# Kernel optimization log

Measured on AMD Instinct MI355X. Metric: run time of the kernel, lower is better.

The kernel has to match this reference:

```python
import jax, jax.numpy as jnp
import numpy as np


def setup_inputs() -> dict:
    key = jax.random.key(0)
    k1, = jax.random.split(key, 1)
    N, H, C, T = 4, 16, 64, 2048
    qkv = jax.random.normal(k1, (N, 3 * H * C, T), dtype=jnp.float32)
    mask = jnp.ones((N, T), dtype=jnp.float32)
    return {"qkv": qkv, "mask": mask, "n_heads": H}


def reference(qkv, mask, n_heads):
    bs, width, length = qkv.shape
    ch = width // (3 * n_heads)
    # [bs*H, 3*ch, T] -> split into q, k, v each [bs*H, ch, T]
    qkv_r = qkv.reshape(bs * n_heads, ch * 3, length)
    q, k, v = qkv_r[:, :ch], qkv_r[:, ch:2 * ch], qkv_r[:, 2 * ch:]
    scale = 1.0 / (ch ** 0.25)  # scale applied to both q and k, as in original
    weight = jnp.einsum('bct,bcs->bts', q * scale, k * scale)  # [bs*H, T, T]
    weight = jax.nn.softmax(weight.astype(jnp.float32), axis=-1).astype(qkv.dtype)
    # torch mask.repeat(n_heads, 1).unsqueeze(1) == tile over leading dim -> [bs*H, 1, T]
    mask_r = jnp.tile(mask, (n_heads, 1))[:, None, :]
    weight = weight * mask_r  # post-softmax multiply (faithful to original)
    a = jnp.einsum('bts,bcs->bct', weight, v)  # [bs*H, ch, T]
    return a.reshape(bs, -1, length)
```

## Files before the change

### kernel.cpp

```cpp
#include <hip/hip_runtime.h>
#include <hip/hip_bf16.h>

typedef __attribute__((ext_vector_type(4))) float f32x4;
typedef __attribute__((ext_vector_type(2))) float f32x2;
typedef __attribute__((ext_vector_type(8))) short s16x8;
typedef __attribute__((ext_vector_type(4))) short s16x4;

constexpr int T_SEQ = 2048;
constexpr int D = 64;
constexpr int H = 16;
constexpr int QBLK = 128;
constexpr int KVBLK = 64;
constexpr int NTHREADS = 512;
constexpr float LOG2E = 1.44269504088896340736f;

__device__ __forceinline__ short f2bf(float f) {
  return (short)__builtin_bit_cast(unsigned short, __float2bfloat16(f));
}

__device__ __forceinline__ float fast_exp2(float x) {
#if __has_builtin(__builtin_amdgcn_exp2f)
  return __builtin_amdgcn_exp2f(x);
#else
  return exp2f(x);
#endif
}

__device__ __forceinline__ int swz(int row, int colByte) {
  return row * 128 + (colByte ^ ((row & 7) << 4));
}

__global__ __launch_bounds__(NTHREADS, 6)
void attn_kernel(const float* __restrict__ qkv, const float* __restrict__ mask,
                 float* __restrict__ out) {
  __shared__ __align__(16) char smem[40960];
  char* Qc = smem;
  char* Kc = smem;
  char* Vc = smem + 8192;
  char* Pc = smem + 16384;
  float* maskLds = (float*)(smem + 32768);

  const int tid = threadIdx.x;
  int flat = blockIdx.y * 16 + blockIdx.x;
  flat = (flat & 7) * 128 + (flat >> 3);
  const int qt = flat & 15;
  const int bh = flat >> 4;
  const int b = bh >> 4, h = bh & 15;

  const size_t headBase = ((size_t)b * (3 * H * D) + (size_t)h * (3 * D)) * T_SEQ;
  const float* gQ = qkv + headBase;
  const float* gK = gQ + (size_t)D * T_SEQ;
  const float* gV = gQ + (size_t)(2 * D) * T_SEQ;
  const float* gM = mask + (size_t)(bh & 3) * T_SEQ;

  *(f32x4*)&maskLds[tid * 4] = *(const f32x4*)&gM[tid * 4];
  {
    const int sb = (tid & 31) * 4;
    const int cb = (tid >> 5) * 4;
    const int q0 = qt * QBLK;
    const float qscale = 0.125f * LOG2E;
    f32x4 r[4];
#pragma unroll
    for (int j = 0; j < 4; ++j)
      r[j] = *(const f32x4*)(gQ + (size_t)(cb + j) * T_SEQ + q0 + sb);
#pragma unroll
    for (int i = 0; i < 4; ++i) {
      s16x4 w;
#pragma unroll
      for (int j = 0; j < 4; ++j) w[j] = f2bf(r[j][i] * qscale);
      *(s16x4*)(Qc + swz(sb + i, 2 * cb)) = w;
    }
  }
  __syncthreads();

  const int wave = tid >> 6, lane = tid & 63;
  const int lg = lane >> 4, lid = lane & 15;

  s16x8 aq[2];
#pragma unroll
  for (int ko = 0; ko < 2; ++ko)
    aq[ko] = *(const s16x8*)(Qc + swz(wave * 16 + lid, 16 * lg + 64 * ko));

  float m0 = -1e30f, l0 = 0.0f;
  f32x4 accO[4];
#pragma unroll
  for (int ct = 0; ct < 4; ++ct) accO[ct] = (f32x4){0.f, 0.f, 0.f, 0.f};

  char* Pw = Pc + wave * 2048;

  for (int s0 = 0; s0 < T_SEQ; s0 += KVBLK) {
    __syncthreads();
    if (tid < 256) {
      const int sb = 2 * (tid & 31);
      const int cb = 8 * (tid >> 5);
      f32x2 r[8];
#pragma unroll
      for (int j = 0; j < 8; ++j)
        r[j] = *(const f32x2*)(gK + (size_t)(cb + j) * T_SEQ + s0 + sb);
#pragma unroll
      for (int i = 0; i < 2; ++i) {
        s16x8 w;
#pragma unroll
        for (int j = 0; j < 8; ++j) w[j] = f2bf(r[j][i]);
        *(s16x8*)(Kc + swz(sb + i, 2 * cb)) = w;
      }
    } else {
      const int t2 = tid - 256;
      const int c = t2 >> 2;
      const int sbase = 16 * (t2 & 3);
      f32x4 r[4], mk[4];
#pragma unroll
      for (int j = 0; j < 4; ++j) {
        r[j] = *(const f32x4*)(gV + (size_t)c * T_SEQ + s0 + sbase + 4 * j);
        mk[j] = *(const f32x4*)&maskLds[s0 + sbase + 4 * j];
      }
      s16x8 w0, w1;
#pragma unroll
      for (int j = 0; j < 8; ++j) w0[j] = f2bf(r[j >> 2][j & 3] * mk[j >> 2][j & 3]);
#pragma unroll
      for (int j = 0; j < 8; ++j)
        w1[j] = f2bf(r[2 + (j >> 2)][j & 3] * mk[2 + (j >> 2)][j & 3]);
      *(s16x8*)(Vc + swz(c, 2 * sbase)) = w0;
      *(s16x8*)(Vc + swz(c, 2 * sbase + 16)) = w1;
    }
    __syncthreads();

    f32x4 accST[4];
#pragma unroll
    for (int nt = 0; nt < 4; ++nt) accST[nt] = (f32x4){0.f, 0.f, 0.f, 0.f};
    __builtin_amdgcn_s_setprio(1);
#pragma unroll
    for (int ko = 0; ko < 2; ++ko) {
#pragma unroll
      for (int nt = 0; nt < 4; ++nt) {
        s16x8 ak = *(const s16x8*)(Kc + swz(nt * 16 + lid, 16 * lg + 64 * ko));
        accST[nt] = __builtin_amdgcn_mfma_f32_16x16x32_bf16(ak, aq[ko], accST[nt], 0, 0, 0);
      }
    }
    __builtin_amdgcn_s_setprio(0);

    float mx[4];
#pragma unroll
    for (int nt = 0; nt < 4; ++nt)
      mx[nt] = fmaxf(fmaxf(accST[nt][0], accST[nt][1]),
                     fmaxf(accST[nt][2], accST[nt][3]));
    float tm = fmaxf(fmaxf(mx[0], mx[1]), fmaxf(mx[2], mx[3]));
    tm = fmaxf(tm, __shfl_xor(tm, 16));
    tm = fmaxf(tm, __shfl_xor(tm, 32));
    if (!__all(tm - m0 <= 11.5416f)) {
      const float nm = fmaxf(m0, tm);
      const float sc = fast_exp2(m0 - nm);
      m0 = nm;
      l0 *= sc;
#pragma unroll
      for (int ct = 0; ct < 4; ++ct) {
#pragma unroll
        for (int r = 0; r < 4; ++r) accO[ct][r] *= sc;
      }
    }
    float p[4][4], ps[4];
#pragma unroll
    for (int nt = 0; nt < 4; ++nt) {
#pragma unroll
      for (int r = 0; r < 4; ++r) p[nt][r] = fast_exp2(accST[nt][r] - m0);
      ps[nt] = (p[nt][0] + p[nt][1]) + (p[nt][2] + p[nt][3]);
    }
    float rs = (ps[0] + ps[1]) + (ps[2] + ps[3]);
    rs += __shfl_xor(rs, 16);
    rs += __shfl_xor(rs, 32);
    l0 += rs;

#pragma unroll
    for (int nt = 0; nt < 4; ++nt) {
      s16x4 w;
#pragma unroll
      for (int r = 0; r < 4; ++r) w[r] = f2bf(p[nt][r]);
      *(s16x4*)(Pw + swz(lid, 32 * nt + 8 * lg)) = w;
    }

    __builtin_amdgcn_s_setprio(1);
#pragma unroll
    for (int ko = 0; ko < 2; ++ko) {
      s16x8 bp = *(const s16x8*)(Pw + swz(lid, 64 * ko + 16 * lg));
#pragma unroll
      for (int ct = 0; ct < 4; ++ct) {
        s16x8 av = *(const s16x8*)(Vc + swz(ct * 16 + lid, 64 * ko + 16 * lg));
        accO[ct] = __builtin_amdgcn_mfma_f32_16x16x32_bf16(av, bp, accO[ct], 0, 0, 0);
      }
    }
    __builtin_amdgcn_s_setprio(0);
  }

  const float rcp = 1.0f / l0;
  const int qcol = qt * QBLK + wave * 16 + lid;
#pragma unroll
  for (int ct = 0; ct < 4; ++ct) {
#pragma unroll
    for (int r = 0; r < 4; ++r) {
      const int c = 16 * ct + 4 * lg + r;
      out[((size_t)(b * (H * D) + h * D + c)) * T_SEQ + qcol] = accO[ct][r] * rcp;
    }
  }
}

extern "C" void kernel_launch(void* const* d_in, const int* in_sizes, int n_in,
                              void* d_out, int out_size, void* d_ws, size_t ws_size,
                              hipStream_t stream) {
  const float* qkv = (const float*)d_in[0];
  const float* mask = (const float*)d_in[1];
  float* out = (float*)d_out;
  dim3 grid(T_SEQ / QBLK, 64);
  attn_kernel<<<grid, NTHREADS, 0, stream>>>(qkv, mask, out);
}
```

Measured before the change: 277.1 us.

## Prefetch next K/V tile into registers during attention compute

Result: slower. 398.1 us (+43.7%).

```diff
diff --git a/kernel.cpp b/kernel.cpp
--- a/kernel.cpp
+++ b/kernel.cpp
@@ -11,6 +11,7 @@
 constexpr int H = 16;
 constexpr int QBLK = 128;
 constexpr int KVBLK = 64;
+constexpr int NT = T_SEQ / KVBLK;
 constexpr int NTHREADS = 512;
 constexpr float LOG2E = 1.44269504088896340736f;
 
@@ -53,6 +54,17 @@
   const float* gV = gQ + (size_t)(2 * D) * T_SEQ;
   const float* gM = mask + (size_t)(bh & 3) * T_SEQ;
 
+  const bool isK = tid < 256;
+  const int t2 = tid & 255;
+  const int ksb = 2 * (t2 & 31);
+  const int kcb = 8 * (t2 >> 5);
+  const int vc = t2 >> 2;
+  const int vsb = 16 * (t2 & 3);
+  const float* stagBase = isK ? (gK + (size_t)kcb * T_SEQ + ksb)
+                              : (gV + (size_t)vc * T_SEQ + vsb);
+  const int sstride = isK ? T_SEQ : 2;
+  f32x2 stg[8];
+
   *(f32x4*)&maskLds[tid * 4] = *(const f32x4*)&gM[tid * 4];
   {
     const int sb = (tid & 31) * 4;
@@ -81,6 +93,10 @@
   for (int ko = 0; ko < 2; ++ko)
     aq[ko] = *(const s16x8*)(Qc + swz(wave * 16 + lid, 16 * lg + 64 * ko));
 
+#pragma unroll
+  for (int j = 0; j < 8; ++j)
+    stg[j] = *(const f32x2*)(stagBase + j * sstride);
+
   float m0 = -1e30f, l0 = 0.0f;
   f32x4 accO[4];
 #pragma unroll
@@ -88,42 +104,40 @@
 
   char* Pw = Pc + wave * 2048;
 
+  __syncthreads();
+
   for (int s0 = 0; s0 < T_SEQ; s0 += KVBLK) {
-    __syncthreads();
-    if (tid < 256) {
-      const int sb = 2 * (tid & 31);
-      const int cb = 8 * (tid >> 5);
-      f32x2 r[8];
-#pragma unroll
-      for (int j = 0; j < 8; ++j)
-        r[j] = *(const f32x2*)(gK + (size_t)(cb + j) * T_SEQ + s0 + sb);
+    if (isK) {
 #pragma unroll
       for (int i = 0; i < 2; ++i) {
         s16x8 w;
 #pragma unroll
-        for (int j = 0; j < 8; ++j) w[j] = f2bf(r[j][i]);
-        *(s16x8*)(Kc + swz(sb + i, 2 * cb)) = w;
+        for (int j = 0; j < 8; ++j) w[j] = f2bf(stg[j][i]);
+        *(s16x8*)(Kc + swz(ksb + i, 2 * kcb)) = w;
       }
     } else {
-      const int t2 = tid - 256;
-      const int c = t2 >> 2;
-      const int sbase = 16 * (t2 & 3);
-      f32x4 r[4], mk[4];
-#pragma unroll
-      for (int j = 0; j < 4; ++j) {
-        r[j] = *(const f32x4*)(gV + (size_t)c * T_SEQ + s0 + sbase + 4 * j);
-        mk[j] = *(const f32x4*)&maskLds[s0 + sbase + 4 * j];
-      }
+      f32x4 mk[4];
+#pragma unroll
+      for (int i = 0; i < 4; ++i)
+        mk[i] = *(const f32x4*)&maskLds[s0 + vsb + 4 * i];
       s16x8 w0, w1;
 #pragma unroll
-      for (int j = 0; j < 8; ++j) w0[j] = f2bf(r[j >> 2][j & 3] * mk[j >> 2][j & 3]);
-#pragma unroll
       for (int j = 0; j < 8; ++j)
-        w1[j] = f2bf(r[2 + (j >> 2)][j & 3] * mk[2 + (j >> 2)][j & 3]);
-      *(s16x8*)(Vc + swz(c, 2 * sbase)) = w0;
-      *(s16x8*)(Vc + swz(c, 2 * sbase + 16)) = w1;
+        w0[j] = f2bf(stg[j >> 1][j & 1] * mk[j >> 2][j & 3]);
+#pragma unroll
+      for (int j = 0; j < 8; ++j)
+        w1[j] = f2bf(stg[4 + (j >> 1)][j & 1] * mk[2 + (j >> 2)][j & 3]);
+      *(s16x8*)(Vc + swz(vc, 2 * vsb)) = w0;
+      *(s16x8*)(Vc + swz(vc, 2 * vsb + 16)) = w1;
     }
     __syncthreads();
+
+    if (s0 + KVBLK < T_SEQ) {
+      const float* src = stagBase + (s0 + KVBLK);
+#pragma unroll
+      for (int j = 0; j < 8; ++j)
+        stg[j] = *(const f32x2*)(src + j * sstride);
+    }
 
     f32x4 accST[4];
 #pragma unroll
@@ -189,6 +203,8 @@
       }
     }
     __builtin_amdgcn_s_setprio(0);
+
+    __syncthreads();
   }
 
   const float rcp = 1.0f / l0;
```
